# Kernel optimization log

Measured on AMD Instinct MI355X. Metric: run time of the kernel, lower is better.

The kernel has to match this reference:

```python
import jax, jax.numpy as jnp
import numpy as np

N, E, B = 10000, 60000, 4
NODE_IN, EDGE_IN, COND_IN, SCALE_IN = 6, 6, 10, 4
H, KW, OUT = 64, 256, 1
NUM_LAYERS = 3


def _lin(key, fan_in, fan_out):
    return jax.random.normal(key, (fan_in, fan_out), jnp.float32) / np.sqrt(fan_in).astype(np.float32)


def setup_inputs() -> dict:
    key = jax.random.key(0)
    ks = jax.random.split(key, 16)
    return {
        "x": jax.random.normal(ks[0], (N, NODE_IN), jnp.float32),
        "edge_attr": jax.random.normal(ks[1], (E, EDGE_IN), jnp.float32),
        "conditions": jax.random.normal(ks[2], (B, COND_IN), jnp.float32),
        "scale": jax.random.normal(ks[3], (B, SCALE_IN), jnp.float32),
        "edge_index": jax.random.randint(ks[4], (2, E), 0, N, dtype=jnp.int32),
        "batch": jnp.sort(jax.random.randint(ks[5], (N,), 0, B, dtype=jnp.int32)),
        # node encoder
        "nW1": _lin(ks[6], NODE_IN, H), "nb1": jnp.zeros((H,), jnp.float32),
        "nW2": _lin(ks[7], H, H), "nb2": jnp.zeros((H,), jnp.float32),
        # condition encoder
        "cW1": _lin(ks[8], COND_IN + SCALE_IN, H), "cb1": jnp.zeros((H,), jnp.float32),
        "cW2": _lin(ks[9], H, H), "cb2": jnp.zeros((H,), jnp.float32),
        # kernel network (DenseNet [EDGE_IN+H, KW//2, KW, H*H])
        "kW1": _lin(ks[10], EDGE_IN + H, KW // 2), "kb1": jnp.zeros((KW // 2,), jnp.float32),
        "kW2": _lin(ks[11], KW // 2, KW), "kb2": jnp.zeros((KW,), jnp.float32),
        "kW3": _lin(ks[12], KW, H * H), "kb3": jnp.zeros((H * H,), jnp.float32),
        # NNConv root weight + bias
        "root": _lin(ks[13], H, H), "conv_bias": jnp.zeros((H,), jnp.float32),
        # output head
        "oW": _lin(ks[14], H, OUT), "ob": jnp.zeros((OUT,), jnp.float32),
    }


def reference(x, edge_attr, conditions, scale, edge_index, batch,
              nW1, nb1, nW2, nb2, cW1, cb1, cW2, cb2,
              kW1, kb1, kW2, kb2, kW3, kb3, root, conv_bias, oW, ob):
    # node + condition encoders
    h = jax.nn.relu(x @ nW1 + nb1) @ nW2 + nb2                                   # [N,H]
    u = jax.nn.relu(jnp.concatenate([conditions, scale], 1) @ cW1 + cb1) @ cW2 + cb2  # [B,H]

    src, dst = edge_index[0], edge_index[1]
    # per-edge conditioned attributes
    ea = jnp.concatenate([edge_attr, u[batch[src]]], axis=1)                     # [E,EDGE_IN+H]
    # kernel network -> per-edge H x H weight (same every layer, compute once)
    k = jax.nn.relu(ea @ kW1 + kb1)
    k = jax.nn.relu(k @ kW2 + kb2)
    w = (k @ kW3 + kb3).reshape(E, H, H)                                          # [E,H,H]

    # mean-aggregation degree (clamped to >=1, matching scatter_mean semantics)
    deg = jnp.maximum(jax.ops.segment_sum(jnp.ones((E,), x.dtype), dst, num_segments=N), 1.0)

    for _ in range(NUM_LAYERS):
        msg = jnp.einsum('ei,eio->eo', h[src], w)                                 # gather + bmm
        agg = jax.ops.segment_sum(msg, dst, num_segments=N) / deg[:, None]        # scatter-mean
        h = jax.nn.relu(agg + h @ root + conv_bias)

    out = h @ oW + ob                                                             # [N,OUT]
    return out, u
```

## Files before the change

kernel.cpp:

```cpp
#include <hip/hip_runtime.h>
#include <hip/hip_fp16.h>

#define N_NODES 10000
#define N_EDGES 60000
#define EPAD    60032
#define CSPLIT  4
#define CT_PER  16

typedef _Float16 f16;
typedef f16 f16x8 __attribute__((ext_vector_type(8)));
typedef float f32x4 __attribute__((ext_vector_type(4)));

__global__ void k_node_enc(const float* __restrict__ x, const float* __restrict__ W1,
                           const float* __restrict__ b1, const float* __restrict__ W2,
                           const float* __restrict__ b2, float* __restrict__ h) {
    __shared__ float t[4][64];
    int g = threadIdx.x >> 6, j = threadIdx.x & 63;
    int node = blockIdx.x * 4 + g;
    float acc = b1[j];
#pragma unroll
    for (int i = 0; i < 6; ++i) acc += x[node * 6 + i] * W1[i * 64 + j];
    t[g][j] = fmaxf(acc, 0.f);
    __syncthreads();
    float acc2 = b2[j];
#pragma unroll
    for (int i = 0; i < 64; ++i) acc2 += t[g][i] * W2[i * 64 + j];
    h[node * 64 + j] = acc2;
}

__global__ void k_cond_enc(const float* __restrict__ cond, const float* __restrict__ scl,
                           const float* __restrict__ W1, const float* __restrict__ b1,
                           const float* __restrict__ W2, const float* __restrict__ b2,
                           float* __restrict__ u, float* __restrict__ out_u) {
    __shared__ float t[4][64];
    __shared__ float cat[4][14];
    int g = threadIdx.x >> 6, j = threadIdx.x & 63;
    if (threadIdx.x < 56) {
        int b = threadIdx.x / 14, i = threadIdx.x % 14;
        cat[b][i] = (i < 10) ? cond[b * 10 + i] : scl[b * 4 + (i - 10)];
    }
    __syncthreads();
    float acc = b1[j];
#pragma unroll
    for (int i = 0; i < 14; ++i) acc += cat[g][i] * W1[i * 64 + j];
    t[g][j] = fmaxf(acc, 0.f);
    __syncthreads();
    float acc2 = b2[j];
#pragma unroll
    for (int i = 0; i < 64; ++i) acc2 += t[g][i] * W2[i * 64 + j];
    u[g * 64 + j] = acc2;
    out_u[g * 64 + j] = acc2;
}

__global__ void k_deg(const int* __restrict__ dst, float* __restrict__ deg) {
    int e = blockIdx.x * 256 + threadIdx.x;
    if (e < N_EDGES) atomicAdd(&deg[dst[e]], 1.0f);
}
__global__ void k_deg_inv(float* __restrict__ deg) {
    int n = blockIdx.x * 256 + threadIdx.x;
    if (n < N_NODES) deg[n] = 1.0f / fmaxf(deg[n], 1.0f);
}

__global__ void k_permute(const float* __restrict__ kW3, const float* __restrict__ kb3,
                          f16* __restrict__ kW3P, float* __restrict__ kb3P) {
    __shared__ float T[256][65];
    int i = blockIdx.x;
    int o = threadIdx.x & 63, kq = threadIdx.x >> 6;
    for (int kk = 0; kk < 64; ++kk) {
        int k = kk * 4 + kq;
        T[k][o] = kW3[(size_t)k * 4096 + i * 64 + o];
    }
    if (threadIdx.x < 64) kb3P[threadIdx.x * 64 + i] = kb3[i * 64 + threadIdx.x];
    __syncthreads();
    int ow = threadIdx.x >> 2, kc = (threadIdx.x & 3) * 64;
    f16* dstp = kW3P + (size_t)(ow * 64 + i) * 256 + kc;
    for (int c = 0; c < 8; ++c) {
        f16x8 v;
#pragma unroll
        for (int jj = 0; jj < 8; ++jj) v[jj] = (f16)T[kc + c * 8 + jj][ow];
        *(f16x8*)(dstp + c * 8) = v;
    }
}

__global__ __launch_bounds__(256) void k_edge12(const float* __restrict__ ea, const int* __restrict__ ei,
                                                const int* __restrict__ batch, const float* __restrict__ u,
                                                const float* __restrict__ W1, const float* __restrict__ b1,
                                                const float* __restrict__ W2, const float* __restrict__ b2,
                                                f16* __restrict__ k2) {
    __shared__ float u_s[256];
    __shared__ float ea_s[16][6];
    __shared__ int b_s[16];
    __shared__ float k1_s[16][128];
    int tid = threadIdx.x;
    int e0 = blockIdx.x * 16;
    u_s[tid] = u[tid];
    if (tid < 96) {
        int e = tid / 6, i = tid % 6;
        int eg = e0 + e;
        ea_s[e][i] = (eg < N_EDGES) ? ea[(size_t)eg * 6 + i] : 0.f;
    }
    if (tid < 16) {
        int eg = e0 + tid;
        b_s[tid] = (eg < N_EDGES) ? batch[ei[eg]] : 0;
    }
    __syncthreads();
    int j = tid & 127;
#pragma unroll 1
    for (int p = 0; p < 8; ++p) {
        int e = p * 2 + (tid >> 7);
        float acc = b1[j];
#pragma unroll
        for (int i = 0; i < 6; ++i) acc += ea_s[e][i] * W1[i * 128 + j];
        const float* ur = u_s + b_s[e] * 64;
#pragma unroll
        for (int i = 0; i < 64; ++i) acc += ur[i] * W1[(6 + i) * 128 + j];
        k1_s[e][j] = fmaxf(acc, 0.f);
    }
    __syncthreads();
    float acc2[16];
#pragma unroll
    for (int e = 0; e < 16; ++e) acc2[e] = b2[tid];
    for (int i = 0; i < 128; ++i) {
        float w = W2[(size_t)i * 256 + tid];
#pragma unroll
        for (int e = 0; e < 16; ++e) acc2[e] += k1_s[e][i] * w;
    }
#pragma unroll
    for (int e = 0; e < 16; ++e) {
        int eg = e0 + e;
        k2[(size_t)eg * 256 + tid] = (f16)((eg < N_EDGES) ? fmaxf(acc2[e], 0.f) : 0.f);
    }
}

__global__ __launch_bounds__(256) void k_fused(const f16* __restrict__ A, const f16* __restrict__ Bm,
                                               const float* __restrict__ kb3P, const float* __restrict__ h,
                                               const int* __restrict__ ei, const float* __restrict__ dinv,
                                               float* __restrict__ agg) {
    __shared__ __align__(16) char lB[32768];
    __shared__ int src_s[128];
    __shared__ int dst_s[128];
    __shared__ float dinv_s[128];
    __shared__ float bias_s[CT_PER * 64];
    int tid = threadIdx.x, wave = tid >> 6, lane = tid & 63;
    int m0 = blockIdx.x * 128;
    int ct0 = blockIdx.y * CT_PER;
    if (tid < 128) {
        int eg = m0 + tid; int s = 0, d = 0; float dv = 0.f;
        if (eg < N_EDGES) { s = ei[eg]; d = ei[N_EDGES + eg]; dv = dinv[d]; }
        src_s[tid] = s; dst_s[tid] = d; dinv_s[tid] = dv;
    }
#pragma unroll
    for (int q = 0; q < CT_PER * 64 / 256; ++q)
        bias_s[q * 256 + tid] = kb3P[ct0 * 64 + q * 256 + tid];
    __syncthreads();
    f16x8 a[2][8];
#pragma unroll
    for (int mf = 0; mf < 2; ++mf) {
        const f16* ap = A + (size_t)(m0 + wave * 32 + mf * 16 + (lane & 15)) * 256 + (lane >> 4) * 8;
#pragma unroll
        for (int ks = 0; ks < 8; ++ks) a[mf][ks] = *(const f16x8*)(ap + ks * 32);
    }
    float hsr[2][4][4];
#pragma unroll
    for (int mf = 0; mf < 2; ++mf)
#pragma unroll
        for (int jj = 0; jj < 4; ++jj) {
            int el = wave * 32 + mf * 16 + (lane >> 4) * 4 + jj;
            const float* hp = h + (size_t)src_s[el] * 64 + (lane & 15);
            float dv = dinv_s[el];
#pragma unroll
            for (int nf = 0; nf < 4; ++nf) hsr[mf][jj][nf] = hp[nf * 16] * dv;
        }
    f16x8 st[8];
    {
        const f16* bp = Bm + (size_t)ct0 * 16384;
#pragma unroll
        for (int q = 0; q < 8; ++q) {
            int v = q * 4 + wave;
            st[q] = *(const f16x8*)(bp + (size_t)(((v >> 3) * 16) + (tid & 15)) * 256 + (v & 7) * 32 + ((tid >> 4) & 3) * 8);
        }
    }
#pragma unroll 1
    for (int ct = ct0; ct < ct0 + CT_PER; ++ct) {
        __syncthreads();
#pragma unroll
        for (int q = 0; q < 8; ++q)
            *(f16x8*)(lB + (q * 256 + tid) * 16) = st[q];
        __syncthreads();
        if (ct + 1 < ct0 + CT_PER) {
            const f16* bp = Bm + (size_t)(ct + 1) * 16384;
#pragma unroll
            for (int q = 0; q < 8; ++q) {
                int v = q * 4 + wave;
                st[q] = *(const f16x8*)(bp + (size_t)(((v >> 3) * 16) + (tid & 15)) * 256 + (v & 7) * 32 + ((tid >> 4) & 3) * 8);
            }
        }
        f32x4 acc[2][4];
#pragma unroll
        for (int nf = 0; nf < 4; ++nf) {
            float bv = bias_s[(ct - ct0) * 64 + nf * 16 + (lane & 15)];
            acc[0][nf] = {bv, bv, bv, bv};
            acc[1][nf] = {bv, bv, bv, bv};
        }
#pragma unroll
        for (int ks = 0; ks < 8; ++ks) {
            f16x8 bf[4];
#pragma unroll
            for (int nf = 0; nf < 4; ++nf)
                bf[nf] = *(const f16x8*)(lB + (nf * 8 + ks) * 1024 + lane * 16);
#pragma unroll
            for (int mf = 0; mf < 2; ++mf)
#pragma unroll
                for (int nf = 0; nf < 4; ++nf)
                    acc[mf][nf] = __builtin_amdgcn_mfma_f32_16x16x32_f16(a[mf][ks], bf[nf], acc[mf][nf], 0, 0, 0);
        }
#pragma unroll
        for (int mf = 0; mf < 2; ++mf)
#pragma unroll
            for (int jj = 0; jj < 4; ++jj) {
                float v = acc[mf][0][jj] * hsr[mf][jj][0] + acc[mf][1][jj] * hsr[mf][jj][1]
                        + acc[mf][2][jj] * hsr[mf][jj][2] + acc[mf][3][jj] * hsr[mf][jj][3];
                v += __shfl_xor(v, 1); v += __shfl_xor(v, 2);
                v += __shfl_xor(v, 4); v += __shfl_xor(v, 8);
                int el = wave * 32 + mf * 16 + (lane >> 4) * 4 + jj;
                if ((lane & 15) == 0 && (m0 + el) < N_EDGES)
                    atomicAdd(&agg[(size_t)dst_s[el] * 64 + ct], v);
            }
    }
}

__global__ void k_update(const float* __restrict__ agg, const float* __restrict__ h,
                         const float* __restrict__ root, const float* __restrict__ bias,
                         float* __restrict__ hn) {
    __shared__ float t[4][64];
    int g = threadIdx.x >> 6, j = threadIdx.x & 63;
    int node = blockIdx.x * 4 + g;
    t[g][j] = h[node * 64 + j];
    __syncthreads();
    float acc = agg[node * 64 + j] + bias[j];
#pragma unroll
    for (int i = 0; i < 64; ++i) acc += t[g][i] * root[i * 64 + j];
    hn[node * 64 + j] = fmaxf(acc, 0.f);
}

__global__ void k_out(const float* __restrict__ h, const float* __restrict__ oW,
                      const float* __restrict__ ob, float* __restrict__ out) {
    int wg = (blockIdx.x * 256 + threadIdx.x) >> 6;
    int lane = threadIdx.x & 63;
    if (wg >= N_NODES) return;
    float p = h[wg * 64 + lane] * oW[lane];
#pragma unroll
    for (int s = 32; s > 0; s >>= 1) p += __shfl_xor(p, s);
    if (lane == 0) out[wg] = p + ob[0];
}

__global__ void k_sentinel(float* out) { out[0] = 1e30f; }

extern "C" void kernel_launch(void* const* d_in, const int* in_sizes, int n_in,
                              void* d_out, int out_size, void* d_ws, size_t ws_size,
                              hipStream_t stream) {
    const float* x          = (const float*)d_in[0];
    const float* edge_attr  = (const float*)d_in[1];
    const float* conditions = (const float*)d_in[2];
    const float* scale      = (const float*)d_in[3];
    const int*   edge_index = (const int*)d_in[4];
    const int*   batch      = (const int*)d_in[5];
    const float* nW1 = (const float*)d_in[6];  const float* nb1 = (const float*)d_in[7];
    const float* nW2 = (const float*)d_in[8];  const float* nb2 = (const float*)d_in[9];
    const float* cW1 = (const float*)d_in[10]; const float* cb1 = (const float*)d_in[11];
    const float* cW2 = (const float*)d_in[12]; const float* cb2 = (const float*)d_in[13];
    const float* kW1 = (const float*)d_in[14]; const float* kb1 = (const float*)d_in[15];
    const float* kW2 = (const float*)d_in[16]; const float* kb2 = (const float*)d_in[17];
    const float* kW3 = (const float*)d_in[18]; const float* kb3 = (const float*)d_in[19];
    const float* root = (const float*)d_in[20]; const float* conv_bias = (const float*)d_in[21];
    const float* oW  = (const float*)d_in[22]; const float* ob  = (const float*)d_in[23];
    float* out = (float*)d_out;

    char* ws = (char*)d_ws;
    size_t off = 0;
    auto alloc = [&](size_t bytes) -> char* {
        char* p = ws + off;
        off += (bytes + 255) & ~(size_t)255;
        return p;
    };
    float* h_a  = (float*)alloc((size_t)N_NODES * 64 * 4);
    float* h_b  = (float*)alloc((size_t)N_NODES * 64 * 4);
    float* agg  = (float*)alloc((size_t)N_NODES * 64 * 4);
    float* u    = (float*)alloc(256 * 4);
    float* deg  = (float*)alloc((size_t)N_NODES * 4);
    f16*   k2   = (f16*)alloc((size_t)EPAD * 256 * 2);
    f16*   kW3P = (f16*)alloc((size_t)4096 * 256 * 2);
    float* kb3P = (float*)alloc(4096 * 4);

    if (off > ws_size) {
        k_sentinel<<<1, 1, 0, stream>>>(out);
        return;
    }

    hipMemsetAsync(deg, 0, (size_t)N_NODES * 4, stream);
    k_node_enc<<<2500, 256, 0, stream>>>(x, nW1, nb1, nW2, nb2, h_a);
    k_cond_enc<<<1, 256, 0, stream>>>(conditions, scale, cW1, cb1, cW2, cb2, u, out + N_NODES);
    k_deg<<<(N_EDGES + 255) / 256, 256, 0, stream>>>(edge_index + N_EDGES, deg);
    k_deg_inv<<<(N_NODES + 255) / 256, 256, 0, stream>>>(deg);
    k_permute<<<64, 256, 0, stream>>>(kW3, kb3, kW3P, kb3P);
    k_edge12<<<EPAD / 16, 256, 0, stream>>>(edge_attr, edge_index, batch, u, kW1, kb1, kW2, kb2, k2);

    float* hc = h_a; float* hn = h_b;
    for (int l = 0; l < 3; ++l) {
        hipMemsetAsync(agg, 0, (size_t)N_NODES * 64 * 4, stream);
        k_fused<<<dim3(EPAD / 128, CSPLIT), 256, 0, stream>>>(k2, kW3P, kb3P, hc, edge_index, deg, agg);
        k_update<<<2500, 256, 0, stream>>>(agg, hc, root, conv_bias, hn);
        float* tmp = hc; hc = hn; hn = tmp;
    }
    k_out<<<2500, 256, 0, stream>>>(hc, oW, ob, out);
}
```

Measured before the change: 913.1 us.

## Double-buffer kernel weights via direct global-to-LDS loads and batch atomics

Pre-permutes kW3 into the exact LDS fragment layout so each output tile can be streamed with global_load_lds straight into a double-buffered shared array, removing the register staging and one barrier per tile. The per-edge reduction now uses a butterfly fold that packs eight row sums across lanes, and each lane issues four consecutive atomics per group of four output columns instead of one lane doing one atomic per column. CT_PER doubles (CSPLIT halves), so each block covers more columns and the grid is smaller. The padded-edge guard on the atomics is removed and LDS use grows, which can lower occupancy.

Result: no change. 896.9 us (-1.8%).

```diff
diff --git a/kernel.cpp b/kernel.cpp
--- a/kernel.cpp
+++ b/kernel.cpp
@@ -4,12 +4,23 @@
 #define N_NODES 10000
 #define N_EDGES 60000
 #define EPAD    60032
-#define CSPLIT  4
-#define CT_PER  16
+#define CSPLIT  2
+#define CT_PER  32
 
 typedef _Float16 f16;
 typedef f16 f16x8 __attribute__((ext_vector_type(8)));
 typedef float f32x4 __attribute__((ext_vector_type(4)));
+
+__device__ __forceinline__ void gload16(const void* g, void* l) {
+    __builtin_amdgcn_global_load_lds((const __attribute__((address_space(1))) unsigned int*)g,
+                                     (__attribute__((address_space(3))) unsigned int*)l, 16, 0, 0);
+}
+
+__device__ __forceinline__ float foldp(float a, float b, int m, int lane) {
+    float x = (lane & m) ? b : a;
+    float y = (lane & m) ? a : b;
+    return x + __shfl_xor(y, m);
+}
 
 __global__ void k_node_enc(const float* __restrict__ x, const float* __restrict__ W1,
                            const float* __restrict__ b1, const float* __restrict__ W2,
@@ -73,12 +84,15 @@
     if (threadIdx.x < 64) kb3P[threadIdx.x * 64 + i] = kb3[i * 64 + threadIdx.x];
     __syncthreads();
     int ow = threadIdx.x >> 2, kc = (threadIdx.x & 3) * 64;
-    f16* dstp = kW3P + (size_t)(ow * 64 + i) * 256 + kc;
+    int nf = i >> 4, rl = i & 15;
     for (int c = 0; c < 8; ++c) {
+        int k0 = kc + c * 8;
+        int ks = k0 >> 5, kg = (k0 >> 3) & 3;
+        int chunk = (nf * 8 + ks) * 64 + kg * 16 + rl;
         f16x8 v;
 #pragma unroll
-        for (int jj = 0; jj < 8; ++jj) v[jj] = (f16)T[kc + c * 8 + jj][ow];
-        *(f16x8*)(dstp + c * 8) = v;
+        for (int jj = 0; jj < 8; ++jj) v[jj] = (f16)T[k0 + jj][ow];
+        *(f16x8*)(kW3P + (size_t)ow * 16384 + chunk * 8) = v;
     }
 }
 
@@ -132,15 +146,15 @@
     }
 }
 
-__global__ __launch_bounds__(256) void k_fused(const f16* __restrict__ A, const f16* __restrict__ Bm,
+__global__ __launch_bounds__(256) void k_fused(const f16* __restrict__ A, const f16* __restrict__ Bf,
                                                const float* __restrict__ kb3P, const float* __restrict__ h,
                                                const int* __restrict__ ei, const float* __restrict__ dinv,
                                                float* __restrict__ agg) {
-    __shared__ __align__(16) char lB[32768];
+    __shared__ __align__(16) f16 lB[2][16384];
+    __shared__ float bias_s[CT_PER * 64];
     __shared__ int src_s[128];
     __shared__ int dst_s[128];
     __shared__ float dinv_s[128];
-    __shared__ float bias_s[CT_PER * 64];
     int tid = threadIdx.x, wave = tid >> 6, lane = tid & 63;
     int m0 = blockIdx.x * 128;
     int ct0 = blockIdx.y * CT_PER;
@@ -152,6 +166,12 @@
 #pragma unroll
     for (int q = 0; q < CT_PER * 64 / 256; ++q)
         bias_s[q * 256 + tid] = kb3P[ct0 * 64 + q * 256 + tid];
+    {
+        const f16* bp = Bf + (size_t)ct0 * 16384;
+#pragma unroll
+        for (int q = 0; q < 8; ++q)
+            gload16(bp + (q * 256 + tid) * 8, &lB[0][(q * 256 + wave * 64) * 8]);
+    }
     __syncthreads();
     f16x8 a[2][8];
 #pragma unroll
@@ -171,61 +191,69 @@
 #pragma unroll
             for (int nf = 0; nf < 4; ++nf) hsr[mf][jj][nf] = hp[nf * 16] * dv;
         }
-    f16x8 st[8];
-    {
-        const f16* bp = Bm + (size_t)ct0 * 16384;
-#pragma unroll
-        for (int q = 0; q < 8; ++q) {
-            int v = q * 4 + wave;
-            st[q] = *(const f16x8*)(bp + (size_t)(((v >> 3) * 16) + (tid & 15)) * 256 + (v & 7) * 32 + ((tid >> 4) & 3) * 8);
+    int cur = 0;
+    float w4[4];
+#pragma unroll 1
+    for (int cto = 0; cto < CT_PER; cto += 4) {
+#pragma unroll
+        for (int q4 = 0; q4 < 4; ++q4) {
+            int ctl = cto + q4;
+            if (ctl + 1 < CT_PER) {
+                const f16* bp = Bf + (size_t)(ct0 + ctl + 1) * 16384;
+#pragma unroll
+                for (int q = 0; q < 8; ++q)
+                    gload16(bp + (q * 256 + tid) * 8, &lB[cur ^ 1][(q * 256 + wave * 64) * 8]);
+            }
+            f32x4 acc[2][4];
+#pragma unroll
+            for (int nf = 0; nf < 4; ++nf) {
+                float bv = bias_s[ctl * 64 + nf * 16 + (lane & 15)];
+                acc[0][nf] = {bv, bv, bv, bv};
+                acc[1][nf] = {bv, bv, bv, bv};
+            }
+            const f16* lb = lB[cur];
+#pragma unroll
+            for (int ks = 0; ks < 8; ++ks) {
+                f16x8 bf[4];
+#pragma unroll
+                for (int nf = 0; nf < 4; ++nf)
+                    bf[nf] = *(const f16x8*)(lb + (nf * 8 + ks) * 512 + lane * 8);
+#pragma unroll
+                for (int mf = 0; mf < 2; ++mf)
+#pragma unroll
+                    for (int nf = 0; nf < 4; ++nf)
+                        acc[mf][nf] = __builtin_amdgcn_mfma_f32_16x16x32_f16(a[mf][ks], bf[nf], acc[mf][nf], 0, 0, 0);
+            }
+            float v[8];
+#pragma unroll
+            for (int mf = 0; mf < 2; ++mf)
+#pragma unroll
+                for (int jj = 0; jj < 4; ++jj)
+                    v[mf * 4 + jj] = acc[mf][0][jj] * hsr[mf][jj][0] + acc[mf][1][jj] * hsr[mf][jj][1]
+                                   + acc[mf][2][jj] * hsr[mf][jj][2] + acc[mf][3][jj] * hsr[mf][jj][3];
+            float t0 = foldp(v[0], v[1], 1, lane);
+            float t1 = foldp(v[2], v[3], 1, lane);
+            float t2 = foldp(v[4], v[5], 1, lane);
+            float t3 = foldp(v[6], v[7], 1, lane);
+            float u0 = foldp(t0, t1, 2, lane);
+            float u1 = foldp(t2, t3, 2, lane);
+            float s0 = foldp(u0, u1, 4, lane);
+            s0 += __shfl_xor(s0, 8);
+            w4[q4] = s0;
+            if (q4 == 3) {
+                if (!(lane & 8)) {
+                    int mf = (lane >> 2) & 1, jj = lane & 3;
+                    int el = wave * 32 + mf * 16 + (lane >> 4) * 4 + jj;
+                    float* ap2 = agg + (size_t)dst_s[el] * 64 + ct0 + cto;
+                    atomicAdd(ap2 + 0, w4[0]);
+                    atomicAdd(ap2 + 1, w4[1]);
+                    atomicAdd(ap2 + 2, w4[2]);
+                    atomicAdd(ap2 + 3, w4[3]);
+                }
+            }
+            cur ^= 1;
+            __syncthreads();
         }
-    }
-#pragma unroll 1
-    for (int ct = ct0; ct < ct0 + CT_PER; ++ct) {
-        __syncthreads();
-#pragma unroll
-        for (int q = 0; q < 8; ++q)
-            *(f16x8*)(lB + (q * 256 + tid) * 16) = st[q];
-        __syncthreads();
-        if (ct + 1 < ct0 + CT_PER) {
-            const f16* bp = Bm + (size_t)(ct + 1) * 16384;
-#pragma unroll
-            for (int q = 0; q < 8; ++q) {
-                int v = q * 4 + wave;
-                st[q] = *(const f16x8*)(bp + (size_t)(((v >> 3) * 16) + (tid & 15)) * 256 + (v & 7) * 32 + ((tid >> 4) & 3) * 8);
-            }
-        }
-        f32x4 acc[2][4];
-#pragma unroll
-        for (int nf = 0; nf < 4; ++nf) {
-            float bv = bias_s[(ct - ct0) * 64 + nf * 16 + (lane & 15)];
-            acc[0][nf] = {bv, bv, bv, bv};
-            acc[1][nf] = {bv, bv, bv, bv};
-        }
-#pragma unroll
-        for (int ks = 0; ks < 8; ++ks) {
-            f16x8 bf[4];
-#pragma unroll
-            for (int nf = 0; nf < 4; ++nf)
-                bf[nf] = *(const f16x8*)(lB + (nf * 8 + ks) * 1024 + lane * 16);
-#pragma unroll
-            for (int mf = 0; mf < 2; ++mf)
-#pragma unroll
-                for (int nf = 0; nf < 4; ++nf)
-                    acc[mf][nf] = __builtin_amdgcn_mfma_f32_16x16x32_f16(a[mf][ks], bf[nf], acc[mf][nf], 0, 0, 0);
-        }
-#pragma unroll
-        for (int mf = 0; mf < 2; ++mf)
-#pragma unroll
-            for (int jj = 0; jj < 4; ++jj) {
-                float v = acc[mf][0][jj] * hsr[mf][jj][0] + acc[mf][1][jj] * hsr[mf][jj][1]
-                        + acc[mf][2][jj] * hsr[mf][jj][2] + acc[mf][3][jj] * hsr[mf][jj][3];
-                v += __shfl_xor(v, 1); v += __shfl_xor(v, 2);
-                v += __shfl_xor(v, 4); v += __shfl_xor(v, 8);
-                int el = wave * 32 + mf * 16 + (lane >> 4) * 4 + jj;
-                if ((lane & 15) == 0 && (m0 + el) < N_EDGES)
-                    atomicAdd(&agg[(size_t)dst_s[el] * 64 + ct], v);
-            }
     }
 }
 
```
